# Performance work log

Measured on AMD Instinct MI355X. Metric: run time of the kernel, lower is better.

## Reference

```python
import jax, jax.numpy as jnp
from jax import lax
import numpy as np

HEADS = 4
FACTOR = 4
EPS = 1e-12  # torch F.normalize eps


def _to_heads(t):
    # b (head c) (h1 fy) (w1 fx) -> b head (c fx fy) (h1 w1)
    b, C, h, w = t.shape
    c = C // HEADS
    h1, w1 = h // FACTOR, w // FACTOR
    t = t.reshape(b, HEADS, c, h1, FACTOR, w1, FACTOR)       # b,head,c,h1,fy,w1,fx
    t = t.transpose(0, 1, 2, 6, 4, 3, 5)                      # b,head,c,fx,fy,h1,w1
    return t.reshape(b, HEADS, c * FACTOR * FACTOR, h1 * w1)


def _from_heads(t, h, w):
    # b head (c fx fy) (h1 w1) -> b (head c) (h1 fy) (w1 fx)
    b = t.shape[0]
    c = t.shape[2] // (FACTOR * FACTOR)
    h1, w1 = h // FACTOR, w // FACTOR
    t = t.reshape(b, HEADS, c, FACTOR, FACTOR, h1, w1)        # b,head,c,fx,fy,h1,w1
    t = t.transpose(0, 1, 2, 5, 4, 6, 3)                      # b,head,c,h1,fy,w1,fx
    return t.reshape(b, HEADS * c, h, w)


def _l2norm(t):
    n = jnp.sqrt(jnp.sum(t * t, axis=-1, keepdims=True))
    return t / jnp.maximum(n, EPS)


def setup_inputs() -> dict:
    key = jax.random.key(0)
    ks = jax.random.split(key, 4)
    dim = 192
    x = jax.random.normal(ks[0], (8, dim, 128, 128), jnp.float32)
    qkv_w = jax.random.normal(ks[1], (3 * dim, dim), jnp.float32) * 0.05
    qkv_b = jnp.zeros((3 * dim,), jnp.float32)
    dw_w = jax.random.normal(ks[2], (3 * dim, 1, 3, 3), jnp.float32) * 0.05
    dw_b = jnp.zeros((3 * dim,), jnp.float32)
    proj_w = jax.random.normal(ks[3], (dim, dim), jnp.float32) * 0.05
    proj_b = jnp.zeros((dim,), jnp.float32)
    temperature = jnp.ones((HEADS, 1, 1), jnp.float32)
    return dict(x=x, qkv_w=qkv_w, qkv_b=qkv_b, dw_w=dw_w, dw_b=dw_b,
                proj_w=proj_w, proj_b=proj_b, temperature=temperature)


def reference(x, qkv_w, qkv_b, dw_w, dw_b, proj_w, proj_b, temperature):
    b, c, h, w = x.shape
    # 1x1 conv qkv
    qkv = jnp.einsum('bchw,oc->bohw', x, qkv_w) + qkv_b[None, :, None, None]
    # 3x3 depthwise conv (groups = 3*dim)
    qkv = lax.conv_general_dilated(
        qkv, dw_w, window_strides=(1, 1), padding=((1, 1), (1, 1)),
        feature_group_count=3 * c,
        dimension_numbers=('NCHW', 'OIHW', 'NCHW')) + dw_b[None, :, None, None]
    q, k, v = jnp.split(qkv, 3, axis=1)
    # H,W are multiples of FACTOR so the module's pad/unpad is a no-op
    q = _l2norm(_to_heads(q))
    k = _l2norm(_to_heads(k))
    v = _to_heads(v)
    # channel-wise attention: [b,head,d,d] with d = (c/head)*16
    attn = jnp.einsum('bhdn,bhen->bhde', q, k) * temperature[None]
    # softmax_1: exp(x) / (sum exp(x) + 1)
    e = jnp.exp(attn)
    attn = e / (jnp.sum(e, axis=-1, keepdims=True) + 1.0)
    out = jnp.einsum('bhde,bhen->bhdn', attn, v)
    out = _from_heads(out, h, w)
    out = jnp.einsum('bchw,oc->bohw', out, proj_w) + proj_b[None, :, None, None]
    return out
```

## Files before the change

kernel.cpp:

```cpp
#include <hip/hip_runtime.h>

#define HW 16384
#define CDIM 192

typedef short bf16x8 __attribute__((ext_vector_type(8)));
typedef short short8 __attribute__((ext_vector_type(8)));
typedef short short4_t __attribute__((ext_vector_type(4)));
typedef float f32x4  __attribute__((ext_vector_type(4)));

__device__ inline void gload_lds16(const void* g, void* l) {
  __builtin_amdgcn_global_load_lds(
      (const __attribute__((address_space(1))) void*)g,
      (__attribute__((address_space(3))) void*)l, 16, 0, 0);
}

__device__ inline short to_bf16_rne(float f) {
  unsigned u = __float_as_uint(f);
  unsigned r = u + 0x7fffu + ((u >> 16) & 1u);
  return (short)(r >> 16);
}

__device__ inline float b2f(short s) {
  return __uint_as_float(((unsigned)(unsigned short)s) << 16);
}

__device__ inline void split_bf16(float a, short& hi, short& lo) {
  unsigned u = __float_as_uint(a);
  hi = (short)(u >> 16);
  float res = a - __uint_as_float(u & 0xffff0000u);
  lo = (short)(__float_as_uint(res) >> 16);
}

__global__ __launch_bounds__(256) void k_zero(float* __restrict__ p, int n) {
  int i = blockIdx.x * 256 + threadIdx.x;
  if (i < n) p[i] = 0.f;
}

__global__ __launch_bounds__(256) void k_split_w(
    const float* __restrict__ W, short* __restrict__ hi,
    short* __restrict__ lo, int n)
{
  int i = blockIdx.x * 256 + threadIdx.x;
  if (i < n) { short h, l; split_bf16(W[i], h, l); hi[i] = h; lo[i] = l; }
}

#define CMM_LOADB(bv, k0)                                                     \
  { _Pragma("unroll")                                                         \
    for (int kk = 0; kk < 2; ++kk) {                                          \
      const int kcg = kg0 + kk * 2;                                           \
      _Pragma("unroll")                                                       \
      for (int j = 0; j < 8; ++j)                                             \
        bv[kk][j] = xf[(size_t)((k0) + kcg * 8 + j) * HW + n0 + px];          \
    } }

#define CMM_STAGEA(k0, b)                                                     \
  { _Pragma("unroll")                                                         \
    for (int ii = 0; ii < 6; ++ii) {                                          \
      const int id = w * 6 + ii, arr = id / 12, mf = id % 12;                 \
      const short* Wp = arr ? Wlo : Whi;                                      \
      const short* g = Wp + (size_t)(m0 + mf * 16 + lr) * CDIM + (k0) + lq * 8; \
      gload_lds16(g, (arr ? Al[b] : Ah[b]) + mf * 512);                       \
    } }

#define CMM_WRITEB(bv, b)                                                     \
  { _Pragma("unroll")                                                         \
    for (int kk = 0; kk < 2; ++kk) {                                          \
      const int kcg = kg0 + kk * 2;                                           \
      short8 h8, l8;                                                          \
      _Pragma("unroll")                                                       \
      for (int j = 0; j < 8; ++j) {                                           \
        short h, l; split_bf16(bv[kk][j], h, l);                              \
        h8[j] = h; l8[j] = l;                                                 \
      }                                                                       \
      *(short8*)&Bh[b][(kcg * 128 + px) * 8] = h8;                            \
      *(short8*)&Bl[b][(kcg * 128 + px) * 8] = l8;                            \
    } }

template <bool SPLITX>
__global__ __launch_bounds__(256) void k_cmm(
    const float* __restrict__ Xf,
    const short* __restrict__ Xhi, const short* __restrict__ Xlo,
    const short* __restrict__ Whi, const short* __restrict__ Wlo,
    const float* __restrict__ bias, void* __restrict__ Outv, int Mtot)
{
  __shared__ short Ah[SPLITX ? 2 : 1][6144], Al[SPLITX ? 2 : 1][6144];
  __shared__ short Bh[SPLITX ? 2 : 1][4096], Bl[SPLITX ? 2 : 1][4096];
  const int t = threadIdx.x, lane = t & 63, w = t >> 6;
  const int lr = lane & 15, lq = lane >> 4;

  int bb, m0, n0;
  if constexpr (SPLITX) {
    const int flat = blockIdx.x;
    const int g = (flat & 7) * (gridDim.x >> 3) + (flat >> 3);
    bb = g / 384;
    const int rem = g % 384;
    m0 = (rem % 3) * 192;
    n0 = (rem / 3) * 128;
  } else {
    bb = blockIdx.z; m0 = blockIdx.y * 192; n0 = blockIdx.x * 128;
  }

  const float* xf = nullptr;
  const short* xh = nullptr;
  const short* xl = nullptr;
  if constexpr (SPLITX) {
    xf = Xf + (size_t)bb * CDIM * HW;
  } else {
    xh = Xhi + (size_t)bb * 24 * HW * 8;
    xl = Xlo + (size_t)bb * 24 * HW * 8;
  }

  f32x4 acc[3][8] = {};

  if constexpr (SPLITX) {
    const int px = t & 127, kg0 = t >> 7;
    float bv[2][8];
    CMM_LOADB(bv, 0);
    CMM_STAGEA(0, 0);
    asm volatile("s_waitcnt vmcnt(6)" ::: "memory");
    __builtin_amdgcn_sched_barrier(0);
    CMM_WRITEB(bv, 0);

    for (int s = 0; s < 6; ++s) {
      const int cur = s & 1;
      asm volatile("s_waitcnt vmcnt(0) lgkmcnt(0)" ::: "memory");
      __builtin_amdgcn_s_barrier();
      __builtin_amdgcn_sched_barrier(0);

      bf16x8 ahf[3], alf[3];
      #pragma unroll
      for (int mi = 0; mi < 3; ++mi) {
        ahf[mi] = *(const bf16x8*)&Ah[cur][(w * 3 + mi) * 512 + lane * 8];
        alf[mi] = *(const bf16x8*)&Al[cur][(w * 3 + mi) * 512 + lane * 8];
      }
      if (s < 5) {
        __builtin_amdgcn_sched_barrier(0);
        CMM_LOADB(bv, (s + 1) << 5);
        CMM_STAGEA((s + 1) << 5, cur ^ 1);
        __builtin_amdgcn_sched_barrier(0);
      }
      __builtin_amdgcn_s_setprio(1);
      #pragma unroll
      for (int j = 0; j < 8; ++j) {
        bf16x8 bhf = *(const bf16x8*)&Bh[cur][(lq * 128 + j * 16 + lr) * 8];
        bf16x8 blf = *(const bf16x8*)&Bl[cur][(lq * 128 + j * 16 + lr) * 8];
        #pragma unroll
        for (int mi = 0; mi < 3; ++mi) {
          acc[mi][j] = __builtin_amdgcn_mfma_f32_16x16x32_bf16(ahf[mi], bhf, acc[mi][j], 0, 0, 0);
          acc[mi][j] = __builtin_amdgcn_mfma_f32_16x16x32_bf16(ahf[mi], blf, acc[mi][j], 0, 0, 0);
          acc[mi][j] = __builtin_amdgcn_mfma_f32_16x16x32_bf16(alf[mi], bhf, acc[mi][j], 0, 0, 0);
        }
      }
      __builtin_amdgcn_s_setprio(0);
      if (s < 5) {
        __builtin_amdgcn_sched_barrier(0);
        asm volatile("s_waitcnt vmcnt(6)" ::: "memory");
        __builtin_amdgcn_sched_barrier(0);
        CMM_WRITEB(bv, cur ^ 1);
      }
    }
  } else {
    for (int k0 = 0; k0 < CDIM; k0 += 32) {
      __syncthreads();
      #pragma unroll
      for (int ii = 0; ii < 6; ++ii) {
        const int id = w * 6 + ii, arr = id / 12, mf = id % 12;
        const short* Wp = arr ? Wlo : Whi;
        const short* g = Wp + (size_t)(m0 + mf * 16 + lr) * CDIM + k0 + lq * 8;
        gload_lds16(g, (arr ? Al[0] : Ah[0]) + mf * 512);
      }
      #pragma unroll
      for (int ii = 0; ii < 4; ++ii) {
        const int id = w * 4 + ii, arr = id >> 3, sub = id & 7;
        const int kc = sub >> 1, half = sub & 1;
        const short* src = arr ? xl : xh;
        const short* g = src + ((size_t)(k0 / 8 + kc) * HW + n0 + half * 64 + lane) * 8;
        gload_lds16(g, (arr ? Bl[0] : Bh[0]) + (kc * 128 + half * 64) * 8);
      }
      __syncthreads();

      bf16x8 ahf[3], alf[3];
      #pragma unroll
      for (int mi = 0; mi < 3; ++mi) {
        ahf[mi] = *(const bf16x8*)&Ah[0][(w * 3 + mi) * 512 + lane * 8];
        alf[mi] = *(const bf16x8*)&Al[0][(w * 3 + mi) * 512 + lane * 8];
      }
      #pragma unroll
      for (int j = 0; j < 8; ++j) {
        bf16x8 bhf = *(const bf16x8*)&Bh[0][(lq * 128 + j * 16 + lr) * 8];
        bf16x8 blf = *(const bf16x8*)&Bl[0][(lq * 128 + j * 16 + lr) * 8];
        #pragma unroll
        for (int mi = 0; mi < 3; ++mi) {
          acc[mi][j] = __builtin_amdgcn_mfma_f32_16x16x32_bf16(ahf[mi], bhf, acc[mi][j], 0, 0, 0);
          acc[mi][j] = __builtin_amdgcn_mfma_f32_16x16x32_bf16(ahf[mi], blf, acc[mi][j], 0, 0, 0);
          acc[mi][j] = __builtin_amdgcn_mfma_f32_16x16x32_bf16(alf[mi], bhf, acc[mi][j], 0, 0, 0);
        }
      }
    }
  }

  #pragma unroll
  for (int mi = 0; mi < 3; ++mi) {
    #pragma unroll
    for (int r = 0; r < 4; ++r) {
      const int m = m0 + (w * 3 + mi) * 16 + lq * 4 + r;
      const float bv2 = bias[m];
      const size_t rowo = ((size_t)bb * Mtot + m) * HW + n0;
      #pragma unroll
      for (int j = 0; j < 8; ++j) {
        const int n = j * 16 + lr;
        if constexpr (SPLITX) {
          ((short*)Outv)[rowo + n] = to_bf16_rne(acc[mi][j][r] + bv2);
        } else {
          ((float*)Outv)[rowo + n] = acc[mi][j][r] + bv2;
        }
      }
    }
  }
}

__global__ __launch_bounds__(256) void k_dw(
    const short* __restrict__ tmp,
    const float* __restrict__ dww, const float* __restrict__ dwb,
    short* __restrict__ Qb, short* __restrict__ Kb,
    short* __restrict__ Vt, int b0)
{
  __shared__ short img[16384];
  __shared__ short dwout[16 * 1040];
  __shared__ float sums[16][64];
  __shared__ float rednorm[16];

  const int gc = blockIdx.x, lb = blockIdx.y, b = b0 + lb;
  const int sel = gc / CDIM, chl = gc % CDIM;
  const int head = chl / 48, c = chl % 48;
  const short* gimg = tmp + ((size_t)lb * 576 + gc) * HW;
  const int t = threadIdx.x;

  #pragma unroll
  for (int cch = 0; cch < 8; ++cch)
    gload_lds16(gimg + cch * 2048 + t * 8, img + cch * 2048 + t * 8);

  float wgt[9];
  #pragma unroll
  for (int i = 0; i < 9; ++i) wgt[i] = dww[gc * 9 + i];
  const float bias = dwb[gc];

  asm volatile("s_waitcnt vmcnt(0)" ::: "memory");
  __syncthreads();

  const int fy = (t >> 4) & 3;
  float sqp[4] = {0.f, 0.f, 0.f, 0.f};

  for (int i = 0; i < 8; ++i) {
    const int p8 = i * 2048 + t * 8;
    const int h = p8 >> 7, w0 = p8 & 127;
    float win[3][10];
    #pragma unroll
    for (int dy = 0; dy < 3; ++dy) {
      const int r = h + dy - 1;
      if (r < 0 || r > 127) {
        #pragma unroll
        for (int q = 0; q < 10; ++q) win[dy][q] = 0.f;
      } else {
        const short* rp = img + r * 128 + w0;
        short8 c8 = *(const short8*)rp;
        win[dy][0] = (w0 > 0) ? b2f(rp[-1]) : 0.f;
        #pragma unroll
        for (int q = 0; q < 8; ++q) win[dy][1 + q] = b2f(c8[q]);
        win[dy][9] = (w0 < 120) ? b2f(rp[8]) : 0.f;
      }
    }
    const int na = (h >> 2) * 32 + (w0 >> 2);
    #pragma unroll
    for (int fx = 0; fx < 4; ++fx) {
      float a0 = bias, a1 = bias;
      #pragma unroll
      for (int dy = 0; dy < 3; ++dy)
        #pragma unroll
        for (int dx = 0; dx < 3; ++dx) {
          a0 = fmaf(win[dy][fx + dx], wgt[dy * 3 + dx], a0);
          a1 = fmaf(win[dy][4 + fx + dx], wgt[dy * 3 + dx], a1);
        }
      sqp[fx] = fmaf(a0, a0, sqp[fx]);
      sqp[fx] = fmaf(a1, a1, sqp[fx]);
      *(unsigned*)&dwout[(fx * 4 + fy) * 1040 + na] =
          ((unsigned)(unsigned short)to_bf16_rne(a1) << 16) |
          (unsigned short)to_bf16_rne(a0);
    }
  }

  if (sel < 2) {
    const int slot = (t & 15) | ((t >> 6) << 4);
    #pragma unroll
    for (int fx = 0; fx < 4; ++fx) sums[fx * 4 + fy][slot] = sqp[fx];
    __syncthreads();
    const int row = t >> 4, i16 = t & 15;
    float v = sums[row][i16] + sums[row][i16 + 16] + sums[row][i16 + 32] + sums[row][i16 + 48];
    __syncthreads();
    sums[row][i16] = v;
    __syncthreads();
    if (t < 16) {
      float s = 0.f;
      #pragma unroll
      for (int j = 0; j < 16; ++j) s += sums[t][j];
      rednorm[t] = fmaxf(sqrtf(s), 1e-12f);
    }
  } else {
    __syncthreads();
  }
  __syncthreads();

  if (sel == 2) {
    #pragma unroll
    for (int j = 0; j < 4; ++j) {
      const int n = t + j * 256;
      short8 v0, v1;
      #pragma unroll
      for (int rr = 0; rr < 8; ++rr) v0[rr] = dwout[rr * 1040 + n];
      #pragma unroll
      for (int rr = 0; rr < 8; ++rr) v1[rr] = dwout[(rr + 8) * 1040 + n];
      const size_t o = ((size_t)(b * 4 + head) * 1024 + n) * 768 + c * 16;
      *(short8*)&Vt[o] = v0;
      *(short8*)&Vt[o + 8] = v1;
    }
    return;
  }

  short* dst = (sel == 0) ? Qb : Kb;
  #pragma unroll
  for (int rr = 0; rr < 16; ++rr) {
    const float inv = 1.0f / rednorm[rr];
    const size_t rowoff = ((size_t)(b * 4 + head) * 768 + c * 16 + rr) * 1024;
    #pragma unroll
    for (int j = 0; j < 2; ++j) {
      const int n2 = j * 512 + t * 2;
      const unsigned pk = *(const unsigned*)&dwout[rr * 1040 + n2];
      const float v0 = b2f((short)(pk & 0xffffu)) * inv;
      const float v1 = b2f((short)(pk >> 16)) * inv;
      *(unsigned*)&dst[rowoff + n2] =
          ((unsigned)(unsigned short)to_bf16_rne(v1) << 16) | (unsigned short)to_bf16_rne(v0);
    }
  }
}

__global__ __launch_bounds__(512) void k_qk(
    const short* __restrict__ Qb, const short* __restrict__ Kbf,
    const float* __restrict__ temp,
    short* __restrict__ E, float* __restrict__ Sums)
{
  __shared__ short lds[3][14336];
  const int t = threadIdx.x, lane = t & 63, w = t >> 6;
  const int lr = lane & 15, lq = lane >> 4;

  const int flat = blockIdx.x;
  const int g = (flat & 7) * 48 + (flat >> 3);
  const int bh = g / 12, tile = g % 12;
  const int m0 = (tile / 3) * 192, n0 = (tile % 3) * 256;
  const size_t base = (size_t)bh * 768 * 1024;

  f32x4 acc[6][4] = {};
  const int wm = (w >> 2) * 6, wn = (w & 3) * 4;

  const short* gsrc[4]; size_t goff[4]; int gdst[4]; bool gok[4];
  #pragma unroll
  for (int ii = 0; ii < 4; ++ii) {
    const int id = w * 4 + ii;
    gok[ii] = (id < 28);
    const bool isq = (id < 12);
    gsrc[ii] = isq ? Qb : Kbf;
    const int row = isq ? (m0 + id * 16) : (n0 + (id - 12) * 16);
    goff[ii] = base + (size_t)(row + lr) * 1024 + lq * 8;
    gdst[ii] = (id < 28 ? id : 0) * 512;
  }
  #define QK_STAGE(buf, k0)                                                   \
    { _Pragma("unroll")                                                       \
      for (int ii = 0; ii < 4; ++ii)                                          \
        if (gok[ii]) gload_lds16(gsrc[ii] + goff[ii] + (k0), &lds[buf][gdst[ii]]); }

  QK_STAGE(0, 0);
  QK_STAGE(1, 32);

  for (int step = 0; step < 32; ++step) {
    const int cur = step % 3;
    if (step == 31) { asm volatile("s_waitcnt vmcnt(0)" ::: "memory"); }
    else            { asm volatile("s_waitcnt vmcnt(4)" ::: "memory"); }
    __builtin_amdgcn_s_barrier();
    __builtin_amdgcn_sched_barrier(0);

    bf16x8 ah[6], bf_[4];
    #pragma unroll
    for (int i = 0; i < 6; ++i)
      ah[i] = *(const bf16x8*)&lds[cur][(wm + i) * 512 + lane * 8];
    #pragma unroll
    for (int j = 0; j < 4; ++j)
      bf_[j] = *(const bf16x8*)&lds[cur][(12 + wn + j) * 512 + lane * 8];

    if (step < 30) QK_STAGE((step + 2) % 3, (step + 2) << 5);

    asm volatile("s_waitcnt lgkmcnt(0)" ::: "memory");
    __builtin_amdgcn_sched_barrier(0);
    __builtin_amdgcn_s_setprio(1);
    #pragma unroll
    for (int i = 0; i < 6; ++i)
      #pragma unroll
      for (int j = 0; j < 4; ++j)
        acc[i][j] = __builtin_amdgcn_mfma_f32_16x16x32_bf16(ah[i], bf_[j], acc[i][j], 0, 0, 0);
    __builtin_amdgcn_s_setprio(0);
    __builtin_amdgcn_sched_barrier(0);
  }
  #undef QK_STAGE

  const float tp = temp[bh & 3];
  float* Srow = Sums + bh * 768;
  short* Ep = E + (size_t)bh * 768 * 768;
  #pragma unroll
  for (int i = 0; i < 6; ++i) {
    #pragma unroll
    for (int r = 0; r < 4; ++r) {
      const int m = m0 + (w >> 2) * 96 + i * 16 + lq * 4 + r;
      short* erow = Ep + (size_t)m * 768 + n0 + (w & 3) * 64;
      float rs = 0.f;
      #pragma unroll
      for (int j = 0; j < 4; ++j) {
        const float e = expf(acc[i][j][r] * tp);
        rs += e;
        erow[j * 16 + lr] = to_bf16_rne(e);
      }
      rs += __shfl_xor(rs, 1);
      rs += __shfl_xor(rs, 2);
      rs += __shfl_xor(rs, 4);
      rs += __shfl_xor(rs, 8);
      if (lr == 0) atomicAdd(&Srow[m], rs);
    }
  }
}

__global__ __launch_bounds__(512) void k_av(
    const short* __restrict__ Ebf, const short* __restrict__ Vtb,
    const float* __restrict__ Sums,
    short* __restrict__ Phi, short* __restrict__ Plo)
{
  __shared__ short lds[3][16384];
  const int t = threadIdx.x, lane = t & 63, w = t >> 6;
  const int lr = lane & 15, lq = lane >> 4;

  const int flat = blockIdx.x;
  const int g = (flat & 7) * 48 + (flat >> 3);
  const int bh = g / 12, tile = g % 12;
  const int m0 = (tile / 4) * 256, n0 = (tile % 4) * 256;
  const int head = bh & 3, b = bh >> 2;
  const short* Sp = Ebf + (size_t)bh * 768 * 768;
  const short* Vp = Vtb + (size_t)bh * 1024 * 768;

  f32x4 acc[8][4] = {};
  const int wm = (w >> 2) * 8, wn = (w & 3) * 4;

  const short* gsrc[4]; size_t goff[4]; int gdst[4];
  #pragma unroll
  for (int ii = 0; ii < 4; ++ii) {
    const int id = w * 4 + ii;
    const int arr = id >> 4, s = id & 15;
    gsrc[ii] = arr ? Vp : Sp;
    const int row = (arr ? n0 : m0) + s * 16;
    goff[ii] = (size_t)(row + lr) * 768 + lq * 8;
    gdst[ii] = id * 512;
  }
  #define AV_STAGE(buf, k0)                                                   \
    { _Pragma("unroll")                                                       \
      for (int ii = 0; ii < 4; ++ii)                                          \
        gload_lds16(gsrc[ii] + goff[ii] + (k0), &lds[buf][gdst[ii]]); }

  AV_STAGE(0, 0);
  AV_STAGE(1, 32);

  for (int step = 0; step < 24; ++step) {
    const int cur = step % 3;
    if (step == 23) { asm volatile("s_waitcnt vmcnt(0)" ::: "memory"); }
    else            { asm volatile("s_waitcnt vmcnt(4)" ::: "memory"); }
    __builtin_amdgcn_s_barrier();
    __builtin_amdgcn_sched_barrier(0);

    bf16x8 ea[8], vb[4];
    #pragma unroll
    for (int i = 0; i < 8; ++i)
      ea[i] = *(const bf16x8*)&lds[cur][(wm + i) * 512 + lane * 8];
    #pragma unroll
    for (int j = 0; j < 4; ++j)
      vb[j] = *(const bf16x8*)&lds[cur][(16 + wn + j) * 512 + lane * 8];

    if (step < 22) AV_STAGE((step + 2) % 3, (step + 2) << 5);

    asm volatile("s_waitcnt lgkmcnt(0)" ::: "memory");
    __builtin_amdgcn_sched_barrier(0);
    __builtin_amdgcn_s_setprio(1);
    #pragma unroll
    for (int i = 0; i < 8; ++i)
      #pragma unroll
      for (int j = 0; j < 4; ++j)
        acc[i][j] = __builtin_amdgcn_mfma_f32_16x16x32_bf16(ea[i], vb[j], acc[i][j], 0, 0, 0);
    __builtin_amdgcn_s_setprio(0);
    __builtin_amdgcn_sched_barrier(0);
  }
  #undef AV_STAGE

  const float* Srow = Sums + bh * 768;
  float invv[8][4];
  #pragma unroll
  for (int i = 0; i < 8; ++i)
    #pragma unroll
    for (int r = 0; r < 4; ++r) {
      const int d = m0 + (w >> 2) * 128 + i * 16 + lq * 4 + r;
      invv[i][r] = 1.0f / (Srow[d] + 1.0f);
    }
  #pragma unroll
  for (int i = 0; i < 8; ++i)
    #pragma unroll
    for (int j = 0; j < 4; ++j)
      #pragma unroll
      for (int r = 0; r < 4; ++r)
        acc[i][j][r] *= invv[i][r];

  short* stg = &lds[0][0];
  const int kcp0 = head * 6 + (m0 >> 7);
  const int myc = w >> 2;

  #pragma unroll
  for (int a = 0; a < 2; ++a) {
    #pragma unroll
    for (int c = 0; c < 2; ++c) {
      __syncthreads();
      if (myc == c) {
        #pragma unroll
        for (int j = 0; j < 4; ++j) {
          const int nl = (w & 3) * 64 + j * 16 + lr;
          #pragma unroll
          for (int r = 0; r < 4; ++r) {
            short8 s8;
            #pragma unroll
            for (int i = 0; i < 8; ++i) {
              const float v = acc[i][j][r];
              const unsigned u = __float_as_uint(v);
              if (a == 0) {
                s8[i] = (short)(u >> 16);
              } else {
                const float res = v - __uint_as_float(u & 0xffff0000u);
                s8[i] = (short)(__float_as_uint(res) >> 16);
              }
            }
            const int loff = (((nl >> 5) * 4 + r) * 128 + (nl & 31) * 4 + lq) * 8;
            *(short8*)&stg[loff] = s8;
          }
        }
      }
      __syncthreads();
      short* dst = (a ? Plo : Phi) +
                   ((size_t)(b * 24 + kcp0 + c) * HW + n0 * 16) * 8;
      #pragma unroll
      for (int it = 0; it < 8; ++it) {
        const int idx = it * 4096 + t * 8;
        *(short8*)&dst[idx] = *(const short8*)&stg[idx];
      }
    }
  }
}

extern "C" void kernel_launch(void* const* d_in, const int* in_sizes, int n_in,
                              void* d_out, int out_size, void* d_ws, size_t ws_size,
                              hipStream_t stream) {
  const float* x      = (const float*)d_in[0];
  const float* qkv_w  = (const float*)d_in[1];
  const float* qkv_b  = (const float*)d_in[2];
  const float* dw_w   = (const float*)d_in[3];
  const float* dw_b   = (const float*)d_in[4];
  const float* proj_w = (const float*)d_in[5];
  const float* proj_b = (const float*)d_in[6];
  const float* temp   = (const float*)d_in[7];
  float* out = (float*)d_out;

  float* F = (float*)d_ws;
  const size_t M25 = (size_t)8 * CDIM * HW;
  short* Qb  = (short*)F;
  short* Plo = Qb + M25;
  short* Kb  = (short*)(F + M25);
  short* Vt  = Kb + M25;
  short* Ebf = (short*)(F + 2 * M25);
  short* Phi = Qb;

  short* tmpf = Ebf;
  const size_t ebfBytes  = (size_t)32 * 768 * 768 * 2;
  const size_t baseBytes = 2 * M25 * 4;
  const size_t wsTailBytes = 294912 * 2 + 32 * 768 * 4 + 256;
  int bpi = 2;
  for (int cand = 8; cand >= 2; cand >>= 1) {
    const size_t tmpfBytes = (size_t)cand * 576 * HW * 2;
    const size_t need = baseBytes + (tmpfBytes > ebfBytes ? tmpfBytes : ebfBytes)
                      + wsTailBytes;
    if (ws_size >= need) { bpi = cand; break; }
  }
  const size_t tmpfBytes = (size_t)bpi * 576 * HW * 2;
  short* WS = (short*)((char*)d_ws + baseBytes +
                       (tmpfBytes > ebfBytes ? tmpfBytes : ebfBytes));
  short* Wq_hi = WS;
  short* Wq_lo = WS + 110592;
  short* Wp_hi = WS + 221184;
  short* Wp_lo = WS + 258048;
  float* Sums  = (float*)(WS + 294912);

  k_split_w<<<dim3(432), 256, 0, stream>>>(qkv_w, Wq_hi, Wq_lo, 110592);
  k_split_w<<<dim3(144), 256, 0, stream>>>(proj_w, Wp_hi, Wp_lo, 36864);
  k_zero<<<dim3(96), 256, 0, stream>>>(Sums, 32 * 768);

  for (int b0 = 0; b0 < 8; b0 += bpi) {
    k_cmm<true><<<dim3(384 * bpi), 256, 0, stream>>>(
        x + (size_t)b0 * CDIM * HW, nullptr, nullptr,
        Wq_hi, Wq_lo, qkv_b, tmpf, 576);
    k_dw<<<dim3(576, bpi), 256, 0, stream>>>(
        tmpf, dw_w, dw_b, Qb, Kb, Vt, b0);
  }

  k_qk<<<dim3(384), 512, 0, stream>>>(Qb, Kb, temp, Ebf, Sums);
  k_av<<<dim3(384), 512, 0, stream>>>(Ebf, Vt, Sums, Phi, Plo);
  k_cmm<false><<<dim3(128, 1, 8), 256, 0, stream>>>(
      nullptr, Phi, Plo, Wp_hi, Wp_lo, proj_b, out, 192);
}
```

Measured before the change: 584.6 us.

## Prefetch B two stages ahead and stage bf16 epilogue through LDS for vector stores

The qkv 1x1-conv GEMM kernel (SPLITX path) now keeps two register buffers for the fp32 activation tile, so global loads for stage s+2 are issued while stage s computes. The vmcnt waits are retuned to match the deeper queue. The shared-memory arrays are merged into one buffer, which lets the bf16 output tile be staged through LDS and written with 16-byte coalesced stores instead of scattered 2-byte stores. The cost is more registers held live, which can reduce occupancy, plus extra barriers and LDS traffic in the epilogue.

```diff
diff --git a/kernel.cpp b/kernel.cpp
--- a/kernel.cpp
+++ b/kernel.cpp
@@ -59,7 +59,7 @@
       const int id = w * 6 + ii, arr = id / 12, mf = id % 12;                 \
       const short* Wp = arr ? Wlo : Whi;                                      \
       const short* g = Wp + (size_t)(m0 + mf * 16 + lr) * CDIM + (k0) + lq * 8; \
-      gload_lds16(g, (arr ? Al[b] : Ah[b]) + mf * 512);                       \
+      gload_lds16(g, smem + (b) * 20480 + arr * 6144 + mf * 512);             \
     } }
 
 #define CMM_WRITEB(bv, b)                                                     \
@@ -72,8 +72,8 @@
         short h, l; split_bf16(bv[kk][j], h, l);                              \
         h8[j] = h; l8[j] = l;                                                 \
       }                                                                       \
-      *(short8*)&Bh[b][(kcg * 128 + px) * 8] = h8;                            \
-      *(short8*)&Bl[b][(kcg * 128 + px) * 8] = l8;                            \
+      *(short8*)&smem[(b) * 20480 + 12288 + (kcg * 128 + px) * 8] = h8;       \
+      *(short8*)&smem[(b) * 20480 + 16384 + (kcg * 128 + px) * 8] = l8;       \
     } }
 
 template <bool SPLITX>
@@ -83,8 +83,7 @@
     const short* __restrict__ Whi, const short* __restrict__ Wlo,
     const float* __restrict__ bias, void* __restrict__ Outv, int Mtot)
 {
-  __shared__ short Ah[SPLITX ? 2 : 1][6144], Al[SPLITX ? 2 : 1][6144];
-  __shared__ short Bh[SPLITX ? 2 : 1][4096], Bl[SPLITX ? 2 : 1][4096];
+  __shared__ short smem[SPLITX ? 40960 : 20480];
   const int t = threadIdx.x, lane = t & 63, w = t >> 6;
   const int lr = lane & 15, lq = lane >> 4;
 
@@ -114,36 +113,41 @@
 
   if constexpr (SPLITX) {
     const int px = t & 127, kg0 = t >> 7;
-    float bv[2][8];
-    CMM_LOADB(bv, 0);
+    float bvA[2][8], bvB[2][8];
+
+    CMM_LOADB(bvA, 0);
+    asm volatile("s_waitcnt vmcnt(0)" ::: "memory");
+    __builtin_amdgcn_sched_barrier(0);
+    CMM_WRITEB(bvA, 0);
     CMM_STAGEA(0, 0);
-    asm volatile("s_waitcnt vmcnt(6)" ::: "memory");
-    __builtin_amdgcn_sched_barrier(0);
-    CMM_WRITEB(bv, 0);
-
+    CMM_LOADB(bvB, 32);
+
+    #pragma unroll
     for (int s = 0; s < 6; ++s) {
       const int cur = s & 1;
-      asm volatile("s_waitcnt vmcnt(0) lgkmcnt(0)" ::: "memory");
+      if (s == 5) { asm volatile("s_waitcnt vmcnt(0) lgkmcnt(0)" ::: "memory"); }
+      else        { asm volatile("s_waitcnt vmcnt(16) lgkmcnt(0)" ::: "memory"); }
       __builtin_amdgcn_s_barrier();
       __builtin_amdgcn_sched_barrier(0);
 
       bf16x8 ahf[3], alf[3];
       #pragma unroll
       for (int mi = 0; mi < 3; ++mi) {
-        ahf[mi] = *(const bf16x8*)&Ah[cur][(w * 3 + mi) * 512 + lane * 8];
-        alf[mi] = *(const bf16x8*)&Al[cur][(w * 3 + mi) * 512 + lane * 8];
-      }
-      if (s < 5) {
-        __builtin_amdgcn_sched_barrier(0);
-        CMM_LOADB(bv, (s + 1) << 5);
-        CMM_STAGEA((s + 1) << 5, cur ^ 1);
-        __builtin_amdgcn_sched_barrier(0);
-      }
+        ahf[mi] = *(const bf16x8*)&smem[cur * 20480 + (w * 3 + mi) * 512 + lane * 8];
+        alf[mi] = *(const bf16x8*)&smem[cur * 20480 + 6144 + (w * 3 + mi) * 512 + lane * 8];
+      }
+      if (s < 5) { CMM_STAGEA((s + 1) << 5, cur ^ 1); }
+      if (s < 4) {
+        if ((s & 1) == 0) { CMM_LOADB(bvA, (s + 2) << 5); }
+        else              { CMM_LOADB(bvB, (s + 2) << 5); }
+      }
+      __builtin_amdgcn_sched_barrier(0);
+
       __builtin_amdgcn_s_setprio(1);
       #pragma unroll
       for (int j = 0; j < 8; ++j) {
-        bf16x8 bhf = *(const bf16x8*)&Bh[cur][(lq * 128 + j * 16 + lr) * 8];
-        bf16x8 blf = *(const bf16x8*)&Bl[cur][(lq * 128 + j * 16 + lr) * 8];
+        bf16x8 bhf = *(const bf16x8*)&smem[cur * 20480 + 12288 + (lq * 128 + j * 16 + lr) * 8];
+        bf16x8 blf = *(const bf16x8*)&smem[cur * 20480 + 16384 + (lq * 128 + j * 16 + lr) * 8];
         #pragma unroll
         for (int mi = 0; mi < 3; ++mi) {
           acc[mi][j] = __builtin_amdgcn_mfma_f32_16x16x32_bf16(ahf[mi], bhf, acc[mi][j], 0, 0, 0);
@@ -152,12 +156,37 @@
         }
       }
       __builtin_amdgcn_s_setprio(0);
+
       if (s < 5) {
         __builtin_amdgcn_sched_barrier(0);
-        asm volatile("s_waitcnt vmcnt(6)" ::: "memory");
+        if (s < 4) { asm volatile("s_waitcnt vmcnt(22)" ::: "memory"); }
+        else       { asm volatile("s_waitcnt vmcnt(6)"  ::: "memory"); }
         __builtin_amdgcn_sched_barrier(0);
-        CMM_WRITEB(bv, cur ^ 1);
-      }
+        if ((s & 1) == 0) { CMM_WRITEB(bvB, cur ^ 1); }
+        else              { CMM_WRITEB(bvA, cur ^ 1); }
+      }
+    }
+
+    __syncthreads();
+    #pragma unroll
+    for (int mi = 0; mi < 3; ++mi) {
+      #pragma unroll
+      for (int r = 0; r < 4; ++r) {
+        const int ml = (w * 3 + mi) * 16 + lq * 4 + r;
+        const float bv2 = bias[m0 + ml];
+        #pragma unroll
+        for (int j = 0; j < 8; ++j)
+          smem[ml * 128 + j * 16 + lr] = to_bf16_rne(acc[mi][j][r] + bv2);
+      }
+    }
+    __syncthreads();
+    short* outp = (short*)Outv;
+    #pragma unroll
+    for (int it = 0; it < 12; ++it) {
+      const int c = it * 256 + t;
+      const int row = c >> 4, n8 = c & 15;
+      *(short8*)&outp[((size_t)bb * Mtot + m0 + row) * HW + n0 + n8 * 8] =
+          *(const short8*)&smem[c * 8];
     }
   } else {
     for (int k0 = 0; k0 < CDIM; k0 += 32) {
@@ -167,7 +196,7 @@
         const int id = w * 6 + ii, arr = id / 12, mf = id % 12;
         const short* Wp = arr ? Wlo : Whi;
         const short* g = Wp + (size_t)(m0 + mf * 16 + lr) * CDIM + k0 + lq * 8;
-        gload_lds16(g, (arr ? Al[0] : Ah[0]) + mf * 512);
+        gload_lds16(g, smem + arr * 6144 + mf * 512);
       }
       #pragma unroll
       for (int ii = 0; ii < 4; ++ii) {
@@ -175,20 +204,20 @@
         const int kc = sub >> 1, half = sub & 1;
         const short* src = arr ? xl : xh;
         const short* g = src + ((size_t)(k0 / 8 + kc) * HW + n0 + half * 64 + lane) * 8;
-        gload_lds16(g, (arr ? Bl[0] : Bh[0]) + (kc * 128 + half * 64) * 8);
+        gload_lds16(g, smem + 12288 + arr * 4096 + (kc * 128 + half * 64) * 8);
       }
       __syncthreads();
 
       bf16x8 ahf[3], alf[3];
       #pragma unroll
       for (int mi = 0; mi < 3; ++mi) {
-        ahf[mi] = *(const bf16x8*)&Ah[0][(w * 3 + mi) * 512 + lane * 8];
-        alf[mi] = *(const bf16x8*)&Al[0][(w * 3 + mi) * 512 + lane * 8];
+        ahf[mi] = *(const bf16x8*)&smem[(w * 3 + mi) * 512 + lane * 8];
+        alf[mi] = *(const bf16x8*)&smem[6144 + (w * 3 + mi) * 512 + lane * 8];
       }
       #pragma unroll
       for (int j = 0; j < 8; ++j) {
-        bf16x8 bhf = *(const bf16x8*)&Bh[0][(lq * 128 + j * 16 + lr) * 8];
-        bf16x8 blf = *(const bf16x8*)&Bl[0][(lq * 128 + j * 16 + lr) * 8];
+        bf16x8 bhf = *(const bf16x8*)&smem[12288 + (lq * 128 + j * 16 + lr) * 8];
+        bf16x8 blf = *(const bf16x8*)&smem[16384 + (lq * 128 + j * 16 + lr) * 8];
         #pragma unroll
         for (int mi = 0; mi < 3; ++mi) {
           acc[mi][j] = __builtin_amdgcn_mfma_f32_16x16x32_bf16(ahf[mi], bhf, acc[mi][j], 0, 0, 0);
@@ -197,23 +226,17 @@
         }
       }
     }
-  }
-
-  #pragma unroll
-  for (int mi = 0; mi < 3; ++mi) {
-    #pragma unroll
-    for (int r = 0; r < 4; ++r) {
-      const int m = m0 + (w * 3 + mi) * 16 + lq * 4 + r;
-      const float bv2 = bias[m];
-      const size_t rowo = ((size_t)bb * Mtot + m) * HW + n0;
-      #pragma unroll
-      for (int j = 0; j < 8; ++j) {
-        const int n = j * 16 + lr;
-        if constexpr (SPLITX) {
-          ((short*)Outv)[rowo + n] = to_bf16_rne(acc[mi][j][r] + bv2);
-        } else {
-          ((float*)Outv)[rowo + n] = acc[mi][j][r] + bv2;
-        }
+
+    #pragma unroll
+    for (int mi = 0; mi < 3; ++mi) {
+      #pragma unroll
+      for (int r = 0; r < 4; ++r) {
+        const int m = m0 + (w * 3 + mi) * 16 + lq * 4 + r;
+        const float bv2 = bias[m];
+        const size_t rowo = ((size_t)bb * Mtot + m) * HW + n0;
+        #pragma unroll
+        for (int j = 0; j < 8; ++j)
+          ((float*)Outv)[rowo + j * 16 + lr] = acc[mi][j][r] + bv2;
       }
     }
   }
```

Result: slower. 605.2 us (+3.5%).
